# Kernel optimization log

Measured on AMD Instinct MI355X. Metric: run time of the kernel, lower is better.

Reference implementation:

```python
import jax, jax.numpy as jnp
import numpy as np

B = 65536
X_DIM = 32
H_DIM = 128


def setup_inputs() -> dict:
    key = jax.random.key(0)
    ks = jax.random.split(key, 11)
    f_scale = 0.1
    x = jax.random.uniform(ks[0], (B, X_DIM), dtype=jnp.float32)
    z = jax.random.normal(ks[1], (B, X_DIM), dtype=jnp.float32)
    # M: rand*0.2 with zero diagonal (use_mask=True, empty dag_seed)
    M = jax.random.uniform(ks[2], (X_DIM, X_DIM), dtype=jnp.float32) * 0.2
    M = M * (1.0 - jnp.eye(X_DIM, dtype=jnp.float32))
    # per-node input linears fc_i: weight [h, x_dim+1], column i zeroed (1e-16)
    Wi = jax.random.normal(ks[3], (X_DIM, H_DIM, X_DIM + 1), dtype=jnp.float32) * f_scale * 0.1
    col_mask = 1.0 - jnp.eye(X_DIM + 1, dtype=jnp.float32)[:X_DIM]  # [x_dim, x_dim+1]
    Wi = Wi * col_mask[:, None, :] + 1e-16 * (1.0 - col_mask)[:, None, :]
    bi = jax.random.normal(ks[4], (X_DIM, H_DIM), dtype=jnp.float32) * 0.01
    wf = jax.random.normal(ks[5], (X_DIM, H_DIM), dtype=jnp.float32) * f_scale * 0.1
    bf = jax.random.normal(ks[6], (X_DIM,), dtype=jnp.float32) * 0.01
    W1 = jax.random.normal(ks[7], (H_DIM, H_DIM), dtype=jnp.float32) * f_scale * 0.1
    b1 = jax.random.normal(ks[8], (H_DIM,), dtype=jnp.float32) * 0.01
    W2 = jax.random.normal(ks[9], (H_DIM, H_DIM), dtype=jnp.float32) * f_scale * 0.1
    b2 = jax.random.normal(ks[10], (H_DIM,), dtype=jnp.float32) * 0.01
    return {"x": x, "z": z, "M": M, "Wi": Wi, "bi": bi, "wf": wf,
            "bf": bf, "W1": W1, "b1": b1, "W2": W2, "b2": b2}


def reference(x, z, M, Wi, bi, wf, bf, W1, b1, W2, b2):
    x_dim = M.shape[0]
    eye = jnp.eye(x_dim, dtype=x.dtype)

    def step(out, xs):
        m_col, oh, Wi_i, bi_i, wf_i, bf_i, z_i = xs
        # x_masked = out * M[:, i]; x_masked[:, i] = 0
        xm = out * (m_col * (1.0 - oh))                       # [B, x_dim]
        # fc_i: cat([x_masked, z_i]) @ W.T + b, then ReLU
        h = jax.nn.relu(xm @ Wi_i[:, :x_dim].T
                        + z_i[:, None] * Wi_i[:, x_dim]
                        + bi_i)                                # [B, h]
        # shared 2-layer MLP
        h = jax.nn.relu(h @ W1.T + b1)
        h = jax.nn.relu(h @ W2.T + b2)
        val = jax.nn.sigmoid(h @ wf_i + bf_i)                  # [B]
        out = out * (1.0 - oh) + val[:, None] * oh             # out[:, i] = val
        return out, None

    xs = (M.T, eye, Wi, bi, wf, bf, z.T)
    out, _ = jax.lax.scan(step, x, xs)
    return out
```

## Files before the change

kernel.cpp:

```cpp
#include <hip/hip_runtime.h>
#include <math.h>

#define XD 32
#define HD 128

typedef float f32x16 __attribute__((ext_vector_type(16)));
typedef int v2i __attribute__((ext_vector_type(2)));
typedef int i32x8 __attribute__((ext_vector_type(8)));

#if __has_builtin(__builtin_amdgcn_cvt_pk_fp8_f32)
#define HAVE_CVT_FP8 1
#endif

static __device__ __forceinline__ unsigned char f2e4m3(float f){
  if (!(f==f)) return 0x7F;
  unsigned u = __float_as_uint(f);
  unsigned s = (u>>24)&0x80;
  float a = fabsf(f);
  if (a >= 464.f) return (unsigned char)(s|0x7E);
  if (a < 0.0009765625f) return (unsigned char)s;
  int e = (int)((u>>23)&0xFF) - 127;
  if (e < -6){
    int m = (int)rintf(ldexpf(a, 9));
    if (m >= 8) return (unsigned char)(s|0x08);
    return (unsigned char)(s|(unsigned)m);
  }
  int m = (int)rintf(ldexpf(a, 3-e));
  if (m == 16){ ++e; m = 8; }
  if (e > 8) return (unsigned char)(s|0x7E);
  return (unsigned char)(s | (unsigned)((e+7)<<3) | (unsigned)(m-8));
}

template<bool HI>
static __device__ __forceinline__ int cvtpk_fp8(float a, float b, int old){
#ifdef HAVE_CVT_FP8
  return __builtin_amdgcn_cvt_pk_fp8_f32(a, b, old, HI);
#else
  int w = (int)f2e4m3(a) | ((int)f2e4m3(b) << 8);
  return HI ? ((old & 0x0000FFFF) | (w << 16)) : ((old & (int)0xFFFF0000) | w);
#endif
}

static __device__ __forceinline__ void plswap(int &x, int &y){
#if __has_builtin(__builtin_amdgcn_permlane32_swap)
  v2i r = __builtin_amdgcn_permlane32_swap(x, y, false, false);
  x = r[0]; y = r[1];
#else
  unsigned lane = threadIdx.x & 63u;
  int sx = __shfl_xor(x, 32, 64);
  int sy = __shfl_xor(y, 32, 64);
  int nx = (lane < 32) ? x : sy;
  int ny = (lane < 32) ? sx : y;
  x = nx; y = ny;
#endif
}

static __device__ __forceinline__ i32x8 c2mx(const f32x16 &ca, const f32x16 &cb){
  i32x8 fr;
#pragma unroll
  for (int q = 0; q < 4; ++q){
    int x = cvtpk_fp8<false>(fmaxf(ca[q*4+0],0.f), fmaxf(ca[q*4+1],0.f), 0);
    x     = cvtpk_fp8<true >(fmaxf(ca[q*4+2],0.f), fmaxf(ca[q*4+3],0.f), x);
    int y = cvtpk_fp8<false>(fmaxf(cb[q*4+0],0.f), fmaxf(cb[q*4+1],0.f), 0);
    y     = cvtpk_fp8<true >(fmaxf(cb[q*4+2],0.f), fmaxf(cb[q*4+3],0.f), y);
    plswap(x, y);
    fr[q*2]   = x;
    fr[q*2+1] = y;
  }
  return fr;
}

static __device__ __forceinline__ f32x16 mfma_mx(i32x8 a, i32x8 b, f32x16 c){
  return __builtin_amdgcn_mfma_scale_f32_32x32x64_f8f6f4(
           a, b, c, 0, 0, 0, 0x7F7F7F7F, 0, 0x7F7F7F7F);
}

static __device__ __forceinline__ void ld8(const float* __restrict__ p, float* dst){
  float4 a = *(const float4*)p, b = *(const float4*)(p+4);
  dst[0]=a.x; dst[1]=a.y; dst[2]=a.z; dst[3]=a.w;
  dst[4]=b.x; dst[5]=b.y; dst[6]=b.z; dst[7]=b.w;
}

__global__ void prep(const float* __restrict__ Wi, const float* __restrict__ bi,
                     const float* __restrict__ W1, const float* __restrict__ b1,
                     const float* __restrict__ W2, const float* __restrict__ b2,
                     const float* __restrict__ M,  const float* __restrict__ wf,
                     unsigned char* __restrict__ wip, unsigned char* __restrict__ w1p,
                     unsigned char* __restrict__ w2p, unsigned char* __restrict__ wfp,
                     unsigned char* __restrict__ bbp, float* __restrict__ Mt){
  int b = (int)blockIdx.x;
  int l = (int)threadIdx.x;
  int h = l >> 5, cl = l & 31;
  if (b < 384){
    int i = b / 12, r = b % 12, kt = r >> 2, fo = r & 3;
    int row = fo*32 + cl;
    unsigned char bytes[8];
#pragma unroll
    for (int j = 0; j < 8; ++j){
      float v;
      if (kt < 2){
        int k = kt*16 + h*8 + j;
        int src = (k == i) ? XD : k;
        v = 8.f * Wi[((size_t)i*HD + row)*(XD+1) + src];
      } else {
        v = (h==0 && j==0) ? 8.f * bi[(size_t)i*HD + row] : 0.f;
      }
      bytes[j] = f2e4m3(v);
    }
    long v8; __builtin_memcpy(&v8, bytes, 8);
    *(long*)(wip + ((size_t)b*64 + l)*8) = v8;
  } else if (b < 400){
    const float* W = (b < 392) ? W1 : W2;
    unsigned char* dp = (b < 392) ? w1p : w2p;
    int f = (b - 384) & 7;
    int fo = f >> 1, f2 = f & 1;
    int row = fo*32 + cl;
    union { unsigned char bt[32]; int4 v[2]; } u;
#pragma unroll
    for (int j = 0; j < 32; ++j)
      u.bt[j] = f2e4m3(8.f * W[(size_t)row*HD + f2*64 + h*32 + j]);
    *(int4*)(dp + ((size_t)((f*2+0)*64 + l))*16) = u.v[0];
    *(int4*)(dp + ((size_t)((f*2+1)*64 + l))*16) = u.v[1];
  } else if (b < 464){
    int f = b - 400;
    int i = f >> 1, f2 = f & 1;
    union { unsigned char bt[32]; int4 v[2]; } u;
#pragma unroll
    for (int j = 0; j < 32; ++j){
      float v = (cl == 0) ? 64.f * wf[(size_t)i*HD + f2*64 + h*32 + j] : 0.f;
      u.bt[j] = f2e4m3(v);
    }
    *(int4*)(wfp + ((size_t)f*64 + l)*32)      = u.v[0];
    *(int4*)(wfp + ((size_t)f*64 + l)*32 + 16) = u.v[1];
  } else if (b == 464){
#pragma unroll
    for (int t = 0; t < 16; ++t){
      int idx = t*64 + l;
      int i = idx >> 5, k = idx & 31;
      Mt[i*32 + k] = M[k*32 + i];
    }
  } else {
#pragma unroll
    for (int f = 0; f < 8; ++f){
      int fo = f & 3;
      int row = fo*32 + cl;
      float v = (f < 4) ? 64.f * b1[row] : 512.f * b2[row];
      unsigned char bytes[8];
#pragma unroll
      for (int j = 0; j < 8; ++j)
        bytes[j] = (h==0 && j==0) ? f2e4m3(v) : 0;
      long v8; __builtin_memcpy(&v8, bytes, 8);
      *(long*)(bbp + ((size_t)f*64 + l)*8) = v8;
    }
  }
}

static __device__ __forceinline__ void pack_xb(const float (&st)[16], const float (&mtv)[16],
                                               float zvv, int i, bool hm, long (&xb)[2]){
  int xbi[2][2];
#pragma unroll
  for (int kt = 0; kt < 2; ++kt)
#pragma unroll
    for (int d = 0; d < 2; ++d){
      float v0 = st[kt*8+4*d+0]*mtv[kt*8+4*d+0];
      float v1 = st[kt*8+4*d+1]*mtv[kt*8+4*d+1];
      float v2 = st[kt*8+4*d+2]*mtv[kt*8+4*d+2];
      float v3 = st[kt*8+4*d+3]*mtv[kt*8+4*d+3];
      int w = cvtpk_fp8<false>(v0, v1, 0);
      xbi[kt][d] = cvtpk_fp8<true>(v2, v3, w);
    }
  const int kti = i>>4, di = (i>>2)&1, sh = 8*(i&3);
  const int msk = ~(0xFF << sh);
  int pz = cvtpk_fp8<false>(zvv, 0.f, 0) & 0xFF;
  int ins = pz << sh;
#pragma unroll
  for (int kt = 0; kt < 2; ++kt)
#pragma unroll
    for (int d = 0; d < 2; ++d)
      if (kt == kti && d == di){
        int mod = (xbi[kt][d] & msk) | ins;
        xbi[kt][d] = hm ? mod : xbi[kt][d];
      }
#pragma unroll
  for (int kt = 0; kt < 2; ++kt)
    xb[kt] = (long)(((unsigned long)(unsigned)xbi[kt][0]) |
                    ((unsigned long)(unsigned)xbi[kt][1] << 32));
}

static __device__ __forceinline__ i32x8 ld_mx(const unsigned char* __restrict__ p){
  union { int4 h[2]; i32x8 v; } u;
  u.h[0] = *(const int4*)(p);
  u.h[1] = *(const int4*)(p + 16);
  return u.v;
}

static __device__ __forceinline__ i32x8 ld_mx_lds(const int4* base, int f, int lane){
  union { int4 h[2]; i32x8 v; } u;
  u.h[0] = base[(f*2+0)*64 + lane];
  u.h[1] = base[(f*2+1)*64 + lane];
  return u.v;
}

__global__ __launch_bounds__(256) __attribute__((amdgpu_waves_per_eu(2, 2)))
void genkern(const float* __restrict__ x, const float* __restrict__ z,
             const float* __restrict__ bf,
             const unsigned char* __restrict__ wip, const unsigned char* __restrict__ w1p,
             const unsigned char* __restrict__ w2p, const unsigned char* __restrict__ wfp,
             const unsigned char* __restrict__ bbp, const float* __restrict__ Mt,
             float* __restrict__ out)
{
  __shared__ int4 wlds[2048];
  __shared__ long wbias[512];
  __shared__ long wibuf[2][768];

  const int tid  = (int)threadIdx.x;
  const int lane = tid & 63;
  const int wv   = tid >> 6;
  const int half = lane >> 5, col = lane & 31;
  const long rbase = (long)blockIdx.x * 128 + wv * 32;

#define STAGE_WIP(stepv, parv) do {                                              \
    const unsigned char* _s = wip + (size_t)(stepv)*6144;                        \
    {                                                                            \
      __builtin_amdgcn_global_load_lds(                                          \
        (const __attribute__((address_space(1))) void*)(_s + wv*1024 + lane*16), \
        (__attribute__((address_space(3))) void*)((char*)&wibuf[parv][0] + wv*1024), \
        16, 0, 0);                                                               \
    }                                                                            \
    if (wv < 2){                                                                 \
      __builtin_amdgcn_global_load_lds(                                          \
        (const __attribute__((address_space(1))) void*)(_s + (4+wv)*1024 + lane*16), \
        (__attribute__((address_space(3))) void*)((char*)&wibuf[parv][0] + (4+wv)*1024), \
        16, 0, 0);                                                               \
    }                                                                            \
  } while(0)

  {
    const int4* s1 = (const int4*)w1p;
    const int4* s2 = (const int4*)w2p;
#pragma unroll
    for (int t = 0; t < 4; ++t)
      wlds[t*256 + tid] = s1[t*256 + tid];
#pragma unroll
    for (int t = 0; t < 4; ++t)
      wlds[1024 + t*256 + tid] = s2[t*256 + tid];
#pragma unroll
    for (int t = 0; t < 2; ++t)
      wbias[t*256 + tid] = ((const long*)bbp)[t*256 + tid];
  }
  STAGE_WIP(0, 0);

  float st[16];
#pragma unroll
  for (int kt = 0; kt < 2; ++kt)
    ld8(x + (rbase + col)*XD + kt*16 + half*8, &st[kt*8]);

  __syncthreads();

  f32x16 zro;
#pragma unroll
  for (int q = 0; q < 16; ++q) zro[q] = 0.f;

  const long bconst = (half == 0) ? 0x38L : 0L;

  i32x8 wfx[2];
  wfx[0] = ld_mx(wfp + ((size_t)0*64 + lane)*32);
  wfx[1] = ld_mx(wfp + ((size_t)1*64 + lane)*32);
  float zA = z[(rbase + col)*XD + 0];

#pragma unroll 1
  for (int i = 0; i < XD; ++i){
    const int ip = (i + 1) & (XD - 1);
    const int c = i & 1;
    const bool hm = (half == ((i>>3)&1));
    const int slot_i = ((i>>4)<<3) | (i&7);
    const float bfv = bf[i];

    STAGE_WIP(ip, c ^ 1);

    float mtv[16];
#pragma unroll
    for (int kt = 0; kt < 2; ++kt)
      ld8(Mt + i*32 + kt*16 + half*8, &mtv[kt*8]);

    long xb[2];
    pack_xb(st, mtv, zA, i, hm, xb);
    zA = z[(rbase + col)*XD + ip];

    f32x16 acc[4];
#pragma unroll
    for (int fo = 0; fo < 4; ++fo){
      long a = wibuf[c][(0*4+fo)*64 + lane];
      acc[fo] = __builtin_amdgcn_mfma_f32_32x32x16_fp8_fp8(a, xb[0], zro, 0,0,0);
    }
#pragma unroll
    for (int fo = 0; fo < 4; ++fo){
      long a = wibuf[c][(1*4+fo)*64 + lane];
      acc[fo] = __builtin_amdgcn_mfma_f32_32x32x16_fp8_fp8(a, xb[1], acc[fo], 0,0,0);
    }
#pragma unroll
    for (int fo = 0; fo < 4; ++fo){
      long a = wibuf[c][(2*4+fo)*64 + lane];
      acc[fo] = __builtin_amdgcn_mfma_f32_32x32x16_fp8_fp8(a, bconst, acc[fo], 0,0,0);
    }

    {
      i32x8 mx0 = c2mx(acc[0], acc[1]);
      i32x8 mx1 = c2mx(acc[2], acc[3]);
#pragma unroll
      for (int fo = 0; fo < 4; ++fo){
        long bfr = wbias[fo*64 + lane];
        acc[fo] = __builtin_amdgcn_mfma_f32_32x32x16_fp8_fp8(bfr, bconst, zro, 0,0,0);
      }
#pragma unroll
      for (int fo = 0; fo < 4; ++fo){
        i32x8 w = ld_mx_lds(wlds, fo*2+0, lane);
        acc[fo] = mfma_mx(w, mx0, acc[fo]);
      }
#pragma unroll
      for (int fo = 0; fo < 4; ++fo){
        i32x8 w = ld_mx_lds(wlds, fo*2+1, lane);
        acc[fo] = mfma_mx(w, mx1, acc[fo]);
      }
    }

    {
      i32x8 mx0 = c2mx(acc[0], acc[1]);
      i32x8 mx1 = c2mx(acc[2], acc[3]);
#pragma unroll
      for (int fo = 0; fo < 4; ++fo){
        long bfr = wbias[(4+fo)*64 + lane];
        acc[fo] = __builtin_amdgcn_mfma_f32_32x32x16_fp8_fp8(bfr, bconst, zro, 0,0,0);
      }
#pragma unroll
      for (int fo = 0; fo < 4; ++fo){
        i32x8 w = ld_mx_lds(wlds, 8 + fo*2+0, lane);
        acc[fo] = mfma_mx(w, mx0, acc[fo]);
      }
#pragma unroll
      for (int fo = 0; fo < 4; ++fo){
        i32x8 w = ld_mx_lds(wlds, 8 + fo*2+1, lane);
        acc[fo] = mfma_mx(w, mx1, acc[fo]);
      }
    }

    {
      i32x8 mx0 = c2mx(acc[0], acc[1]);
      i32x8 mx1 = c2mx(acc[2], acc[3]);
      f32x16 e = mfma_mx(wfx[0], mx0, zro);
      e = mfma_mx(wfx[1], mx1, e);
      float u = e[0];
      float s = __shfl_xor(u, 32, 64);
      float t = half ? s : u;
      float v = 1.f/(1.f + __expf(-(t*(1.f/32768.f) + bfv)));
#pragma unroll
      for (int q = 0; q < 16; ++q)
        if (q == slot_i)
          st[q] = hm ? v : st[q];
    }
    wfx[0] = ld_mx(wfp + ((size_t)(ip*2 + 0)*64 + lane)*32);
    wfx[1] = ld_mx(wfp + ((size_t)(ip*2 + 1)*64 + lane)*32);

    __syncthreads();
  }

#pragma unroll
  for (int kt = 0; kt < 2; ++kt){
    float* p = out + (rbase + col)*XD + kt*16 + half*8;
    float4 a, b;
    a.x = st[kt*8+0]; a.y = st[kt*8+1]; a.z = st[kt*8+2]; a.w = st[kt*8+3];
    b.x = st[kt*8+4]; b.y = st[kt*8+5]; b.z = st[kt*8+6]; b.w = st[kt*8+7];
    *(float4*)p = a;
    *(float4*)(p+4) = b;
  }
#undef STAGE_WIP
}

extern "C" void kernel_launch(void* const* d_in, const int* in_sizes, int n_in,
                              void* d_out, int out_size, void* d_ws, size_t ws_size,
                              hipStream_t stream){
  (void)in_sizes; (void)n_in; (void)out_size; (void)ws_size;
  const float* x  = (const float*)d_in[0];
  const float* z  = (const float*)d_in[1];
  const float* M  = (const float*)d_in[2];
  const float* Wi = (const float*)d_in[3];
  const float* bi = (const float*)d_in[4];
  const float* wf = (const float*)d_in[5];
  const float* bf = (const float*)d_in[6];
  const float* W1 = (const float*)d_in[7];
  const float* b1 = (const float*)d_in[8];
  const float* W2 = (const float*)d_in[9];
  const float* b2 = (const float*)d_in[10];

  unsigned char* wip = (unsigned char*)d_ws;
  unsigned char* w1p = wip + 196608;
  unsigned char* w2p = w1p + 16384;
  unsigned char* wfp = w2p + 16384;
  unsigned char* bbp = wfp + 131072;
  float*         Mt  = (float*)(bbp + 4096);

  prep<<<dim3(466), dim3(64), 0, stream>>>(Wi, bi, W1, b1, W2, b2, M, wf,
                                           wip, w1p, w2p, wfp, bbp, Mt);
  genkern<<<dim3(512), dim3(256), 0, stream>>>(x, z, bf, wip, w1p, w2p, wfp, bbp,
                                               Mt, (float*)d_out);
}
```

Before: 143.8 us.

## Replace per-node fp8 MFMA chain with single MX-scaled MFMA and drop LDS staging

The per-node input linear layer previously ran three 32x32x16 fp8 MFMAs per output tile, with weights staged through a double-buffered LDS area via global_load_lds and a block barrier every step. Now the weights are packed into the 32x32x64 MX layout, including the bias column. Each output tile uses one scaled MFMA, and its operand is built by swapping the packed activations across lane halves. The per-node weights are prefetched directly into registers for the next step, which removes the LDS buffer and the per-iteration __syncthreads. This costs extra register pressure and a register permutation step, and it adds global-load latency on the serial scan path.

```diff
diff --git a/kernel.cpp b/kernel.cpp
--- a/kernel.cpp
+++ b/kernel.cpp
@@ -85,34 +85,33 @@
                      const float* __restrict__ W1, const float* __restrict__ b1,
                      const float* __restrict__ W2, const float* __restrict__ b2,
                      const float* __restrict__ M,  const float* __restrict__ wf,
-                     unsigned char* __restrict__ wip, unsigned char* __restrict__ w1p,
+                     unsigned char* __restrict__ wipx, unsigned char* __restrict__ w1p,
                      unsigned char* __restrict__ w2p, unsigned char* __restrict__ wfp,
                      unsigned char* __restrict__ bbp, float* __restrict__ Mt){
   int b = (int)blockIdx.x;
   int l = (int)threadIdx.x;
   int h = l >> 5, cl = l & 31;
-  if (b < 384){
-    int i = b / 12, r = b % 12, kt = r >> 2, fo = r & 3;
+  if (b < 128){
+    int i = b >> 2, fo = b & 3;
     int row = fo*32 + cl;
-    unsigned char bytes[8];
-#pragma unroll
-    for (int j = 0; j < 8; ++j){
+    union { unsigned char bt[32]; int4 v[2]; } u;
+#pragma unroll
+    for (int j = 0; j < 32; ++j){
       float v;
-      if (kt < 2){
-        int k = kt*16 + h*8 + j;
-        int src = (k == i) ? XD : k;
+      if (h == 0){
+        int src = (j == i) ? XD : j;
         v = 8.f * Wi[((size_t)i*HD + row)*(XD+1) + src];
       } else {
-        v = (h==0 && j==0) ? 8.f * bi[(size_t)i*HD + row] : 0.f;
-      }
-      bytes[j] = f2e4m3(v);
-    }
-    long v8; __builtin_memcpy(&v8, bytes, 8);
-    *(long*)(wip + ((size_t)b*64 + l)*8) = v8;
-  } else if (b < 400){
-    const float* W = (b < 392) ? W1 : W2;
-    unsigned char* dp = (b < 392) ? w1p : w2p;
-    int f = (b - 384) & 7;
+        v = (j == 0) ? 8.f * bi[(size_t)i*HD + row] : 0.f;
+      }
+      u.bt[j] = f2e4m3(v);
+    }
+    *(int4*)(wipx + ((size_t)(i*4+fo)*64 + l)*32)      = u.v[0];
+    *(int4*)(wipx + ((size_t)(i*4+fo)*64 + l)*32 + 16) = u.v[1];
+  } else if (b < 144){
+    const float* W = (b < 136) ? W1 : W2;
+    unsigned char* dp = (b < 136) ? w1p : w2p;
+    int f = (b - 128) & 7;
     int fo = f >> 1, f2 = f & 1;
     int row = fo*32 + cl;
     union { unsigned char bt[32]; int4 v[2]; } u;
@@ -121,8 +120,8 @@
       u.bt[j] = f2e4m3(8.f * W[(size_t)row*HD + f2*64 + h*32 + j]);
     *(int4*)(dp + ((size_t)((f*2+0)*64 + l))*16) = u.v[0];
     *(int4*)(dp + ((size_t)((f*2+1)*64 + l))*16) = u.v[1];
-  } else if (b < 464){
-    int f = b - 400;
+  } else if (b < 208){
+    int f = b - 144;
     int i = f >> 1, f2 = f & 1;
     union { unsigned char bt[32]; int4 v[2]; } u;
 #pragma unroll
@@ -132,7 +131,7 @@
     }
     *(int4*)(wfp + ((size_t)f*64 + l)*32)      = u.v[0];
     *(int4*)(wfp + ((size_t)f*64 + l)*32 + 16) = u.v[1];
-  } else if (b == 464){
+  } else if (b == 208){
 #pragma unroll
     for (int t = 0; t < 16; ++t){
       int idx = t*64 + l;
@@ -155,38 +154,6 @@
   }
 }
 
-static __device__ __forceinline__ void pack_xb(const float (&st)[16], const float (&mtv)[16],
-                                               float zvv, int i, bool hm, long (&xb)[2]){
-  int xbi[2][2];
-#pragma unroll
-  for (int kt = 0; kt < 2; ++kt)
-#pragma unroll
-    for (int d = 0; d < 2; ++d){
-      float v0 = st[kt*8+4*d+0]*mtv[kt*8+4*d+0];
-      float v1 = st[kt*8+4*d+1]*mtv[kt*8+4*d+1];
-      float v2 = st[kt*8+4*d+2]*mtv[kt*8+4*d+2];
-      float v3 = st[kt*8+4*d+3]*mtv[kt*8+4*d+3];
-      int w = cvtpk_fp8<false>(v0, v1, 0);
-      xbi[kt][d] = cvtpk_fp8<true>(v2, v3, w);
-    }
-  const int kti = i>>4, di = (i>>2)&1, sh = 8*(i&3);
-  const int msk = ~(0xFF << sh);
-  int pz = cvtpk_fp8<false>(zvv, 0.f, 0) & 0xFF;
-  int ins = pz << sh;
-#pragma unroll
-  for (int kt = 0; kt < 2; ++kt)
-#pragma unroll
-    for (int d = 0; d < 2; ++d)
-      if (kt == kti && d == di){
-        int mod = (xbi[kt][d] & msk) | ins;
-        xbi[kt][d] = hm ? mod : xbi[kt][d];
-      }
-#pragma unroll
-  for (int kt = 0; kt < 2; ++kt)
-    xb[kt] = (long)(((unsigned long)(unsigned)xbi[kt][0]) |
-                    ((unsigned long)(unsigned)xbi[kt][1] << 32));
-}
-
 static __device__ __forceinline__ i32x8 ld_mx(const unsigned char* __restrict__ p){
   union { int4 h[2]; i32x8 v; } u;
   u.h[0] = *(const int4*)(p);
@@ -204,14 +171,13 @@
 __global__ __launch_bounds__(256) __attribute__((amdgpu_waves_per_eu(2, 2)))
 void genkern(const float* __restrict__ x, const float* __restrict__ z,
              const float* __restrict__ bf,
-             const unsigned char* __restrict__ wip, const unsigned char* __restrict__ w1p,
+             const unsigned char* __restrict__ wipx, const unsigned char* __restrict__ w1p,
              const unsigned char* __restrict__ w2p, const unsigned char* __restrict__ wfp,
              const unsigned char* __restrict__ bbp, const float* __restrict__ Mt,
              float* __restrict__ out)
 {
   __shared__ int4 wlds[2048];
   __shared__ long wbias[512];
-  __shared__ long wibuf[2][768];
 
   const int tid  = (int)threadIdx.x;
   const int lane = tid & 63;
@@ -219,22 +185,6 @@
   const int half = lane >> 5, col = lane & 31;
   const long rbase = (long)blockIdx.x * 128 + wv * 32;
 
-#define STAGE_WIP(stepv, parv) do {                                              \
-    const unsigned char* _s = wip + (size_t)(stepv)*6144;                        \
-    {                                                                            \
-      __builtin_amdgcn_global_load_lds(                                          \
-        (const __attribute__((address_space(1))) void*)(_s + wv*1024 + lane*16), \
-        (__attribute__((address_space(3))) void*)((char*)&wibuf[parv][0] + wv*1024), \
-        16, 0, 0);                                                               \
-    }                                                                            \
-    if (wv < 2){                                                                 \
-      __builtin_amdgcn_global_load_lds(                                          \
-        (const __attribute__((address_space(1))) void*)(_s + (4+wv)*1024 + lane*16), \
-        (__attribute__((address_space(3))) void*)((char*)&wibuf[parv][0] + (4+wv)*1024), \
-        16, 0, 0);                                                               \
-    }                                                                            \
-  } while(0)
-
   {
     const int4* s1 = (const int4*)w1p;
     const int4* s2 = (const int4*)w2p;
@@ -248,7 +198,6 @@
     for (int t = 0; t < 2; ++t)
       wbias[t*256 + tid] = ((const long*)bbp)[t*256 + tid];
   }
-  STAGE_WIP(0, 0);
 
   float st[16];
 #pragma unroll
@@ -263,7 +212,11 @@
 
   const long bconst = (half == 0) ? 0x38L : 0L;
 
+  i32x8 wiA[4];
   i32x8 wfx[2];
+#pragma unroll
+  for (int fo = 0; fo < 4; ++fo)
+    wiA[fo] = ld_mx(wipx + ((size_t)(0*4+fo)*64 + lane)*32);
   wfx[0] = ld_mx(wfp + ((size_t)0*64 + lane)*32);
   wfx[1] = ld_mx(wfp + ((size_t)1*64 + lane)*32);
   float zA = z[(rbase + col)*XD + 0];
@@ -271,38 +224,65 @@
 #pragma unroll 1
   for (int i = 0; i < XD; ++i){
     const int ip = (i + 1) & (XD - 1);
-    const int c = i & 1;
     const bool hm = (half == ((i>>3)&1));
     const int slot_i = ((i>>4)<<3) | (i&7);
     const float bfv = bf[i];
 
-    STAGE_WIP(ip, c ^ 1);
-
     float mtv[16];
 #pragma unroll
     for (int kt = 0; kt < 2; ++kt)
       ld8(Mt + i*32 + kt*16 + half*8, &mtv[kt*8]);
 
-    long xb[2];
-    pack_xb(st, mtv, zA, i, hm, xb);
+    int q[4];
+#pragma unroll
+    for (int kt = 0; kt < 2; ++kt)
+#pragma unroll
+      for (int d = 0; d < 2; ++d){
+        float v0 = st[kt*8+4*d+0]*mtv[kt*8+4*d+0];
+        float v1 = st[kt*8+4*d+1]*mtv[kt*8+4*d+1];
+        float v2 = st[kt*8+4*d+2]*mtv[kt*8+4*d+2];
+        float v3 = st[kt*8+4*d+3]*mtv[kt*8+4*d+3];
+        int w = cvtpk_fp8<false>(v0, v1, 0);
+        q[kt*2+d] = cvtpk_fp8<true>(v2, v3, w);
+      }
+    {
+      const int qi = ((i>>4)<<1) | ((i>>2)&1);
+      const int sh = 8*(i&3);
+      const int msk = ~(0xFF << sh);
+      int pz = cvtpk_fp8<false>(zA, 0.f, 0) & 0xFF;
+      int ins = pz << sh;
+#pragma unroll
+      for (int t = 0; t < 4; ++t)
+        if (t == qi){
+          int mod = (q[t] & msk) | ins;
+          q[t] = hm ? mod : q[t];
+        }
+    }
     zA = z[(rbase + col)*XD + ip];
+    int p[4];
+#pragma unroll
+    for (int t = 0; t < 4; ++t){
+      int a = q[t], b = q[t];
+      plswap(a, b);
+      p[t] = half ? a : b;
+    }
+    i32x8 xmx;
+    xmx[0] = half ? 0x38 : q[0];
+    xmx[1] = half ? 0 : q[1];
+    xmx[2] = half ? 0 : p[0];
+    xmx[3] = half ? 0 : p[1];
+    xmx[4] = half ? 0 : q[2];
+    xmx[5] = half ? 0 : q[3];
+    xmx[6] = half ? 0 : p[2];
+    xmx[7] = half ? 0 : p[3];
 
     f32x16 acc[4];
 #pragma unroll
-    for (int fo = 0; fo < 4; ++fo){
-      long a = wibuf[c][(0*4+fo)*64 + lane];
-      acc[fo] = __builtin_amdgcn_mfma_f32_32x32x16_fp8_fp8(a, xb[0], zro, 0,0,0);
-    }
-#pragma unroll
-    for (int fo = 0; fo < 4; ++fo){
-      long a = wibuf[c][(1*4+fo)*64 + lane];
-      acc[fo] = __builtin_amdgcn_mfma_f32_32x32x16_fp8_fp8(a, xb[1], acc[fo], 0,0,0);
-    }
-#pragma unroll
-    for (int fo = 0; fo < 4; ++fo){
-      long a = wibuf[c][(2*4+fo)*64 + lane];
-      acc[fo] = __builtin_amdgcn_mfma_f32_32x32x16_fp8_fp8(a, bconst, acc[fo], 0,0,0);
-    }
+    for (int fo = 0; fo < 4; ++fo)
+      acc[fo] = mfma_mx(wiA[fo], xmx, zro);
+#pragma unroll
+    for (int fo = 0; fo < 4; ++fo)
+      wiA[fo] = ld_mx(wipx + ((size_t)(ip*4+fo)*64 + lane)*32);
 
     {
       i32x8 mx0 = c2mx(acc[0], acc[1]);
@@ -354,14 +334,12 @@
       float t = half ? s : u;
       float v = 1.f/(1.f + __expf(-(t*(1.f/32768.f) + bfv)));
 #pragma unroll
-      for (int q = 0; q < 16; ++q)
-        if (q == slot_i)
-          st[q] = hm ? v : st[q];
+      for (int qq = 0; qq < 16; ++qq)
+        if (qq == slot_i)
+          st[qq] = hm ? v : st[qq];
     }
     wfx[0] = ld_mx(wfp + ((size_t)(ip*2 + 0)*64 + lane)*32);
     wfx[1] = ld_mx(wfp + ((size_t)(ip*2 + 1)*64 + lane)*32);
-
-    __syncthreads();
   }
 
 #pragma unroll
@@ -373,7 +351,6 @@
     *(float4*)p = a;
     *(float4*)(p+4) = b;
   }
-#undef STAGE_WIP
 }
 
 extern "C" void kernel_launch(void* const* d_in, const int* in_sizes, int n_in,
@@ -392,15 +369,15 @@
   const float* W2 = (const float*)d_in[9];
   const float* b2 = (const float*)d_in[10];
 
-  unsigned char* wip = (unsigned char*)d_ws;
-  unsigned char* w1p = wip + 196608;
-  unsigned char* w2p = w1p + 16384;
-  unsigned char* wfp = w2p + 16384;
-  unsigned char* bbp = wfp + 131072;
-  float*         Mt  = (float*)(bbp + 4096);
-
-  prep<<<dim3(466), dim3(64), 0, stream>>>(Wi, bi, W1, b1, W2, b2, M, wf,
-                                           wip, w1p, w2p, wfp, bbp, Mt);
-  genkern<<<dim3(512), dim3(256), 0, stream>>>(x, z, bf, wip, w1p, w2p, wfp, bbp,
+  unsigned char* wipx = (unsigned char*)d_ws;
+  unsigned char* w1p  = wipx + 262144;
+  unsigned char* w2p  = w1p + 16384;
+  unsigned char* wfp  = w2p + 16384;
+  unsigned char* bbp  = wfp + 131072;
+  float*         Mt   = (float*)(bbp + 4096);
+
+  prep<<<dim3(210), dim3(64), 0, stream>>>(Wi, bi, W1, b1, W2, b2, M, wf,
+                                           wipx, w1p, w2p, wfp, bbp, Mt);
+  genkern<<<dim3(512), dim3(256), 0, stream>>>(x, z, bf, wipx, w1p, w2p, wfp, bbp,
                                                Mt, (float*)d_out);
 }
```

After: 174.5 us. 1.21x slower.

## Load per-step input weights directly into registers, drop LDS double buffer and barrier

Applied to the files above, without the earlier changes.

The per-node input-layer weights were staged into an LDS double buffer with global_load_lds, which needed a block barrier every step. Now each lane loads its 12 fp8 weight fragments straight from global memory into registers, prefetching the next step's fragments right after the current MFMAs. This removes the per-step __syncthreads and the LDS traffic, so waves can run out of step with each other. The cost is about 24 extra VGPRs and redundant global/L2 reads by every wave.

```diff
diff --git a/kernel.cpp b/kernel.cpp
--- a/kernel.cpp
+++ b/kernel.cpp
@@ -211,7 +211,6 @@
 {
   __shared__ int4 wlds[2048];
   __shared__ long wbias[512];
-  __shared__ long wibuf[2][768];
 
   const int tid  = (int)threadIdx.x;
   const int lane = tid & 63;
@@ -219,22 +218,6 @@
   const int half = lane >> 5, col = lane & 31;
   const long rbase = (long)blockIdx.x * 128 + wv * 32;
 
-#define STAGE_WIP(stepv, parv) do {                                              \
-    const unsigned char* _s = wip + (size_t)(stepv)*6144;                        \
-    {                                                                            \
-      __builtin_amdgcn_global_load_lds(                                          \
-        (const __attribute__((address_space(1))) void*)(_s + wv*1024 + lane*16), \
-        (__attribute__((address_space(3))) void*)((char*)&wibuf[parv][0] + wv*1024), \
-        16, 0, 0);                                                               \
-    }                                                                            \
-    if (wv < 2){                                                                 \
-      __builtin_amdgcn_global_load_lds(                                          \
-        (const __attribute__((address_space(1))) void*)(_s + (4+wv)*1024 + lane*16), \
-        (__attribute__((address_space(3))) void*)((char*)&wibuf[parv][0] + (4+wv)*1024), \
-        16, 0, 0);                                                               \
-    }                                                                            \
-  } while(0)
-
   {
     const int4* s1 = (const int4*)w1p;
     const int4* s2 = (const int4*)w2p;
@@ -248,7 +231,6 @@
     for (int t = 0; t < 2; ++t)
       wbias[t*256 + tid] = ((const long*)bbp)[t*256 + tid];
   }
-  STAGE_WIP(0, 0);
 
   float st[16];
 #pragma unroll
@@ -263,7 +245,13 @@
 
   const long bconst = (half == 0) ? 0x38L : 0L;
 
+  long wif[3][4];
   i32x8 wfx[2];
+#pragma unroll
+  for (int kt = 0; kt < 3; ++kt)
+#pragma unroll
+    for (int fo = 0; fo < 4; ++fo)
+      wif[kt][fo] = *(const long*)(wip + (((size_t)(kt*4 + fo))*64 + lane)*8);
   wfx[0] = ld_mx(wfp + ((size_t)0*64 + lane)*32);
   wfx[1] = ld_mx(wfp + ((size_t)1*64 + lane)*32);
   float zA = z[(rbase + col)*XD + 0];
@@ -271,13 +259,10 @@
 #pragma unroll 1
   for (int i = 0; i < XD; ++i){
     const int ip = (i + 1) & (XD - 1);
-    const int c = i & 1;
     const bool hm = (half == ((i>>3)&1));
     const int slot_i = ((i>>4)<<3) | (i&7);
     const float bfv = bf[i];
 
-    STAGE_WIP(ip, c ^ 1);
-
     float mtv[16];
 #pragma unroll
     for (int kt = 0; kt < 2; ++kt)
@@ -289,20 +274,19 @@
 
     f32x16 acc[4];
 #pragma unroll
-    for (int fo = 0; fo < 4; ++fo){
-      long a = wibuf[c][(0*4+fo)*64 + lane];
-      acc[fo] = __builtin_amdgcn_mfma_f32_32x32x16_fp8_fp8(a, xb[0], zro, 0,0,0);
-    }
-#pragma unroll
-    for (int fo = 0; fo < 4; ++fo){
-      long a = wibuf[c][(1*4+fo)*64 + lane];
-      acc[fo] = __builtin_amdgcn_mfma_f32_32x32x16_fp8_fp8(a, xb[1], acc[fo], 0,0,0);
-    }
-#pragma unroll
-    for (int fo = 0; fo < 4; ++fo){
-      long a = wibuf[c][(2*4+fo)*64 + lane];
-      acc[fo] = __builtin_amdgcn_mfma_f32_32x32x16_fp8_fp8(a, bconst, acc[fo], 0,0,0);
-    }
+    for (int fo = 0; fo < 4; ++fo)
+      acc[fo] = __builtin_amdgcn_mfma_f32_32x32x16_fp8_fp8(wif[0][fo], xb[0], zro, 0,0,0);
+#pragma unroll
+    for (int fo = 0; fo < 4; ++fo)
+      acc[fo] = __builtin_amdgcn_mfma_f32_32x32x16_fp8_fp8(wif[1][fo], xb[1], acc[fo], 0,0,0);
+#pragma unroll
+    for (int fo = 0; fo < 4; ++fo)
+      acc[fo] = __builtin_amdgcn_mfma_f32_32x32x16_fp8_fp8(wif[2][fo], bconst, acc[fo], 0,0,0);
+#pragma unroll
+    for (int kt = 0; kt < 3; ++kt)
+#pragma unroll
+      for (int fo = 0; fo < 4; ++fo)
+        wif[kt][fo] = *(const long*)(wip + (((size_t)(ip*12 + kt*4 + fo))*64 + lane)*8);
 
     {
       i32x8 mx0 = c2mx(acc[0], acc[1]);
@@ -360,8 +344,6 @@
     }
     wfx[0] = ld_mx(wfp + ((size_t)(ip*2 + 0)*64 + lane)*32);
     wfx[1] = ld_mx(wfp + ((size_t)(ip*2 + 1)*64 + lane)*32);
-
-    __syncthreads();
   }
 
 #pragma unroll
@@ -373,7 +355,6 @@
     *(float4*)p = a;
     *(float4*)(p+4) = b;
   }
-#undef STAGE_WIP
 }
 
 extern "C" void kernel_launch(void* const* d_in, const int* in_sizes, int n_in,
```

New measurement: 185.6 us. 1.29x slower.
